# Optimization experiments

Measured on AMD Instinct MI355X. Metric: run time of the kernel, lower is better.

Reference implementation:

```python
import jax, jax.numpy as jnp
import numpy as np

N = 100000
IN_C = 128
HID = 32   # 2*out_channels
OUT = 16
NEG_SLOPE = 0.2


def gat_layer(x, src, dst, n, W, a_src, a_dst, b):
    # x: [n, Cin] -> h: [n, Cout]
    h = x @ W
    alpha_s = h @ a_src  # [n]
    alpha_d = h @ a_dst  # [n]
    e = jax.nn.leaky_relu(alpha_s[src] + alpha_d[dst], NEG_SLOPE)  # [E]
    # softmax over edges grouped by destination node (self-loops ensure no empty groups)
    m = jax.ops.segment_max(e, dst, num_segments=n)
    ex = jnp.exp(e - m[dst])
    s = jax.ops.segment_sum(ex, dst, num_segments=n)
    alpha = ex / s[dst]  # [E]
    out = jax.ops.segment_sum(h[src] * alpha[:, None], dst, num_segments=n)
    return out + b


def setup_inputs() -> dict:
    key = jax.random.key(0)
    ks = jax.random.split(key, 16)
    x = jax.random.normal(ks[0], (N, IN_C), dtype=jnp.float32)
    edge_index = jax.random.randint(ks[1], (2, 1600000), 0, N, dtype=jnp.int64)

    def glorot(k, shape):
        fan = shape[0] + (shape[1] if len(shape) > 1 else 1)
        return jax.random.normal(k, shape, dtype=jnp.float32) * jnp.sqrt(2.0 / fan)

    return {
        "x": x,
        "edge_index": edge_index,
        "W1": glorot(ks[2], (IN_C, HID)),
        "a1_src": glorot(ks[3], (HID,)),
        "a1_dst": glorot(ks[4], (HID,)),
        "b1": jnp.zeros((HID,), dtype=jnp.float32),
        "W_mu": glorot(ks[5], (HID, OUT)),
        "a_mu_src": glorot(ks[6], (OUT,)),
        "a_mu_dst": glorot(ks[7], (OUT,)),
        "b_mu": jnp.zeros((OUT,), dtype=jnp.float32),
        "W_ls": glorot(ks[8], (HID, OUT)),
        "a_ls_src": glorot(ks[9], (OUT,)),
        "a_ls_dst": glorot(ks[10], (OUT,)),
        "b_ls": jnp.zeros((OUT,), dtype=jnp.float32),
    }


def reference(x, edge_index, W1, a1_src, a1_dst, b1,
              W_mu, a_mu_src, a_mu_dst, b_mu,
              W_ls, a_ls_src, a_ls_dst, b_ls):
    n = x.shape[0]
    # PyG GATConv default: add self-loops
    loop = jnp.arange(n, dtype=edge_index.dtype)
    src = jnp.concatenate([edge_index[0], loop])
    dst = jnp.concatenate([edge_index[1], loop])

    h = jax.nn.relu(gat_layer(x, src, dst, n, W1, a1_src, a1_dst, b1))
    mu = gat_layer(h, src, dst, n, W_mu, a_mu_src, a_mu_dst, b_mu)
    logstd = gat_layer(h, src, dst, n, W_ls, a_ls_src, a_ls_dst, b_ls)
    return (mu, logstd)
```

## Files before the change

kernel.cpp:

```cpp
#include <hip/hip_runtime.h>
#include <hip/hip_bf16.h>
#include <hip/hip_fp16.h>

typedef unsigned int u32;
typedef unsigned short u16;

__device__ __forceinline__ float lrelu(float v) {
    return v > 0.f ? v : 0.2f * v;
}

__device__ __forceinline__ float4 ldq_h16(const u16* __restrict__ row, int q) {
    uint2 u = ((const uint2*)row)[q];
    __half2 a = *(__half2*)&u.x;
    __half2 b = *(__half2*)&u.y;
    float2 fa = __half22float2(a);
    float2 fb = __half22float2(b);
    return make_float4(fa.x, fa.y, fb.x, fb.y);
}

__device__ __forceinline__ u32 pack2h(float x, float y) {
    __half2 h = __float22half2_rn(make_float2(x, y));
    return *(u32*)&h;
}

#define PCHUNK 4096
#define NW 256

__global__ __launch_bounds__(256) void partition_kernel(
    const int* __restrict__ srcI, const int* __restrict__ dstI,
    u32* __restrict__ pairs, u32* __restrict__ bcur,
    int E, int wsz, int cap)
{
    __shared__ u32 lcount[NW];
    __shared__ u32 lbase[NW];
    int t = threadIdx.x;
    int chunk = blockIdx.x * PCHUNK;
    lcount[t] = 0;
    __syncthreads();
    u32 pk[16]; int wv[16]; u32 rk[16]; bool val[16];
#pragma unroll
    for (int g = 0; g < 4; g++) {
        int i0 = chunk + g * 1024 + 4 * t;
        int4 s4, d4;
        bool v4 = (i0 + 3) < E;
        if (v4) {
            s4 = *(const int4*)&srcI[i0];
            d4 = *(const int4*)&dstI[i0];
        }
        int sv[4] = {s4.x, s4.y, s4.z, s4.w};
        int dv[4] = {d4.x, d4.y, d4.z, d4.w};
#pragma unroll
        for (int j = 0; j < 4; j++) {
            int k = g * 4 + j;
            int i = i0 + j;
            val[k] = i < E;
            if (val[k]) {
                u32 s, d;
                if (v4) { s = (u32)sv[j]; d = (u32)dv[j]; }
                else    { s = (u32)srcI[i]; d = (u32)dstI[i]; }
                wv[k] = d / (u32)wsz;
                u32 dloc = d - (u32)wv[k] * (u32)wsz;
                pk[k] = (dloc << 17) | s;
                rk[k] = atomicAdd(&lcount[wv[k]], 1u);
            }
        }
    }
    __syncthreads();
    if (lcount[t] > 0)
        lbase[t] = atomicAdd(&bcur[t], lcount[t]);
    __syncthreads();
#pragma unroll
    for (int k = 0; k < 16; k++) {
        if (val[k]) {
            u32 pos = lbase[wv[k]] + rk[k];
            if (pos < (u32)cap)
                pairs[(size_t)wv[k] * cap + pos] = pk[k];
        }
    }
}

struct GSm { float xs[64][132]; float Wl[128][32]; float asv[32], adv[32]; };
struct CSm { u32 dw[512], cw[512], ts[256], hb[512]; };

__global__ __launch_bounds__(256) void g1c_kernel(
    const float* __restrict__ x, const float* __restrict__ W,
    const float* __restrict__ a_src, const float* __restrict__ a_dst,
    u16* __restrict__ h16, float* __restrict__ as_, float* __restrict__ ad_,
    const u32* __restrict__ pairs, const u32* __restrict__ bcur,
    u32* __restrict__ rowS, u32* __restrict__ deg, int* __restrict__ srcS,
    u32* __restrict__ perm,
    int n, int wsz, int cap)
{
    __shared__ __align__(16) char smraw[sizeof(GSm)];
    int t = threadIdx.x;

    if ((int)blockIdx.x < NW) {
        CSm& s = *reinterpret_cast<CSm*>(smraw);
        int grp = blockIdx.x;
        int wlo = grp * wsz;
        int wnodes = n - wlo; if (wnodes < 0) wnodes = 0; if (wnodes > wsz) wnodes = wsz;
        u32 cnt = bcur[grp]; if (cnt > (u32)cap) cnt = (u32)cap;
        size_t base = (size_t)grp * cap;

        {
            int wlo_t = t * wsz;
            int wn_t = n - wlo_t; if (wn_t < 0) wn_t = 0; if (wn_t > wsz) wn_t = wsz;
            u32 c_t = bcur[t]; if (c_t > (u32)cap) c_t = (u32)cap;
            s.ts[t] = c_t + (u32)wn_t;
            __syncthreads();
            for (int o = 1; o < NW; o <<= 1) {
                u32 y = (t >= o) ? s.ts[t - o] : 0u;
                __syncthreads();
                s.ts[t] += y;
                __syncthreads();
            }
        }
        u32 wb = s.ts[grp] - (cnt + (u32)wnodes);
        __syncthreads();

        s.dw[t] = 0; s.dw[t + 256] = 0;
        s.hb[t] = 0; s.hb[t + 256] = 0;
        __syncthreads();
        for (u32 i = t; i < cnt; i += 256)
            atomicAdd(&s.dw[pairs[base + i] >> 17], 1u);
        __syncthreads();

        int i0 = 2 * t, i1 = 2 * t + 1;
        u32 e0 = (i0 < wnodes) ? s.dw[i0] + 1u : 0u;
        u32 e1 = (i1 < wnodes) ? s.dw[i1] + 1u : 0u;
        s.ts[t] = e0 + e1;
        __syncthreads();
        for (int o = 1; o < 256; o <<= 1) {
            u32 y = (t >= o) ? s.ts[t - o] : 0u;
            __syncthreads();
            s.ts[t] += y;
            __syncthreads();
        }
        u32 off = wb + s.ts[t] - (e0 + e1);
        if (i0 < wnodes) {
            u32 dgi = s.dw[i0];
            s.cw[i0] = off;
            rowS[wlo + i0] = off;
            deg[wlo + i0] = dgi;
            srcS[off + dgi] = wlo + i0;
        }
        u32 off1 = off + e0;
        if (i1 < wnodes) {
            u32 dgi = s.dw[i1];
            s.cw[i1] = off1;
            rowS[wlo + i1] = off1;
            deg[wlo + i1] = dgi;
            srcS[off1 + dgi] = wlo + i1;
        }
        __syncthreads();

        for (int i = t; i < wnodes; i += 256)
            atomicAdd(&s.hb[s.dw[i] < 511u ? s.dw[i] : 511u], 1u);
        __syncthreads();
        {
            u32 h0 = s.hb[2 * t], h1 = s.hb[2 * t + 1];
            s.ts[t] = h0 + h1;
            __syncthreads();
            for (int o = 1; o < 256; o <<= 1) {
                u32 y = (t >= o) ? s.ts[t - o] : 0u;
                __syncthreads();
                s.ts[t] += y;
                __syncthreads();
            }
            u32 b0 = s.ts[t] - (h0 + h1);
            s.hb[2 * t] = b0;
            s.hb[2 * t + 1] = b0 + h0;
        }
        __syncthreads();
        for (int i = t; i < wnodes; i += 256) {
            u32 dg = s.dw[i] < 511u ? s.dw[i] : 511u;
            u32 pos = atomicAdd(&s.hb[dg], 1u);
            perm[wlo + pos] = (u32)(wlo + i);
        }
        for (int i = wnodes + t; i < wsz; i += 256)
            perm[wlo + i] = 0x7fffffffu;
        __syncthreads();

        for (u32 i = t; i < cnt; i += 256) {
            u32 pr = pairs[base + i];
            u32 pos = atomicAdd(&s.cw[pr >> 17], 1u);
            srcS[pos] = (int)(pr & 0x1FFFFu);
        }
        return;
    }

    GSm& s = *reinterpret_cast<GSm*>(smraw);
    int rb = (blockIdx.x - NW) * 64;

    for (int i = t; i < 4096; i += 256) s.Wl[i >> 5][i & 31] = W[i];
    if (t < 32) { s.asv[t] = a_src[t]; s.adv[t] = a_dst[t]; }
    for (int i = t; i < 2048; i += 256) {
        int row = i >> 5, seg = i & 31;
        float4 v = make_float4(0.f, 0.f, 0.f, 0.f);
        if (rb + row < n)
            v = ((const float4*)(x + (size_t)(rb + row) * 128))[seg];
        int c = seg * 4;
        s.xs[row][c + 0] = v.x; s.xs[row][c + 1] = v.y;
        s.xs[row][c + 2] = v.z; s.xs[row][c + 3] = v.w;
    }
    __syncthreads();

    int tr = t >> 3;
    int tc = t & 7;
    float acc[2][4];
#pragma unroll
    for (int i = 0; i < 2; i++)
#pragma unroll
        for (int j = 0; j < 4; j++) acc[i][j] = 0.f;

#pragma unroll 4
    for (int k = 0; k < 128; k++) {
        float x0 = s.xs[tr][k];
        float x1 = s.xs[tr + 32][k];
        float4 wv = *(const float4*)&s.Wl[k][tc * 4];
        acc[0][0] += x0 * wv.x; acc[0][1] += x0 * wv.y;
        acc[0][2] += x0 * wv.z; acc[0][3] += x0 * wv.w;
        acc[1][0] += x1 * wv.x; acc[1][1] += x1 * wv.y;
        acc[1][2] += x1 * wv.z; acc[1][3] += x1 * wv.w;
    }

#pragma unroll
    for (int i = 0; i < 2; i++) {
        int r = rb + tr + i * 32;
        if (r < n) {
            uint2 p;
            p.x = pack2h(acc[i][0], acc[i][1]);
            p.y = pack2h(acc[i][2], acc[i][3]);
            *(uint2*)&h16[(size_t)r * 32 + tc * 4] = p;
        }
        float ps = 0.f, pd = 0.f;
#pragma unroll
        for (int j = 0; j < 4; j++) {
            int c = tc * 4 + j;
            ps += acc[i][j] * s.asv[c];
            pd += acc[i][j] * s.adv[c];
        }
        for (int m = 1; m < 8; m <<= 1) {
            ps += __shfl_xor(ps, m, 64);
            pd += __shfl_xor(pd, m, 64);
        }
        if (tc == 0 && r < n) { as_[r] = ps; ad_[r] = pd; }
    }
}

__global__ __launch_bounds__(256) void l1g2_kernel(
    const u32* __restrict__ rowS, const u32* __restrict__ deg,
    const int* __restrict__ srcS, const u32* __restrict__ perm,
    const float* __restrict__ as_, const float* __restrict__ ad_,
    const u16* __restrict__ h16, const float* __restrict__ b1,
    const float* __restrict__ Wm, const float* __restrict__ Wl_,
    const float* __restrict__ ams, const float* __restrict__ amd,
    const float* __restrict__ alsb, const float* __restrict__ ald,
    u16* __restrict__ hmhl16, float2* __restrict__ attn2,
    float* __restrict__ amud, float* __restrict__ alsd,
    int n, int ntot)
{
    __shared__ float hs[16][36];
    __shared__ float Wms[32][16], Wls[32][16];
    __shared__ float amsv[16], amdv[16], alsv[16], aldv[16];
    __shared__ int dsl[16];
    int t = threadIdx.x;

    for (int i = t; i < 512; i += 256) {
        Wms[i >> 4][i & 15] = Wm[i];
        Wls[i >> 4][i & 15] = Wl_[i];
    }
    if (t < 16) {
        amsv[t] = ams[t]; amdv[t] = amd[t];
        alsv[t] = alsb[t]; aldv[t] = ald[t];
    }

    int gid = blockIdx.x * 16 + (t >> 4);
    int d = (gid < ntot) ? (int)perm[gid] : 0x7fffffff;
    bool live = (u32)d < (u32)n;
    int l  = t & 15;
    int e2 = l >> 3;
    int q  = l & 7;
    int gb = (t & 63) & 48;

    int beg = 0, end = 0;
    float adv = 0.f;
    if (live) {
        beg = (int)rowS[d];
        end = beg + (int)deg[d] + 1;
        adv = ad_[d];
    }

    float wsum = 0.f;
    float4 acc = make_float4(0.f, 0.f, 0.f, 0.f);

    int tb = beg;
    int full_end = beg + ((end - beg) & ~15);
    for (; tb < full_end; tb += 16) {
        int s = srcS[tb + l];
        float p = __expf(fminf(lrelu(as_[s] + adv), 60.f));
#pragma unroll
        for (int jj = 0; jj < 16; jj += 2) {
            int idx = jj + e2;
            int sj  = __shfl(s, gb + idx, 64);
            float w = __shfl(p, gb + idx, 64);
            wsum += w;
            float4 hv = ldq_h16(h16 + (size_t)sj * 32, q);
            acc.x += w * hv.x; acc.y += w * hv.y;
            acc.z += w * hv.z; acc.w += w * hv.w;
        }
    }
    if (tb < end) {
        int j = tb + l;
        bool valid = j < end;
        int s = valid ? srcS[j] : 0;
        float p = valid ? __expf(fminf(lrelu(as_[s] + adv), 60.f)) : 0.f;
        int cnt = end - tb;
        for (int jj = 0; jj < cnt; jj += 2) {
            int idx = jj + e2;
            int sj  = __shfl(s, gb + idx, 64);
            float w = __shfl(p, gb + idx, 64);
            if (idx >= cnt) w = 0.f;
            wsum += w;
            float4 hv = ldq_h16(h16 + (size_t)sj * 32, q);
            acc.x += w * hv.x; acc.y += w * hv.y;
            acc.z += w * hv.z; acc.w += w * hv.w;
        }
    }
    wsum  += __shfl_xor(wsum, 8, 64);
    acc.x += __shfl_xor(acc.x, 8, 64);
    acc.y += __shfl_xor(acc.y, 8, 64);
    acc.z += __shfl_xor(acc.z, 8, 64);
    acc.w += __shfl_xor(acc.w, 8, 64);

    if (l == 0) dsl[t >> 4] = live ? d : -1;
    if (live && l < 8) {
        float inv = 1.f / wsum;
        float4 r;
        r.x = fmaxf(acc.x * inv + b1[4 * q + 0], 0.f);
        r.y = fmaxf(acc.y * inv + b1[4 * q + 1], 0.f);
        r.z = fmaxf(acc.z * inv + b1[4 * q + 2], 0.f);
        r.w = fmaxf(acc.w * inv + b1[4 * q + 3], 0.f);
        *(float4*)&hs[t >> 4][4 * q] = r;
    }
    __syncthreads();

    int tr = t >> 4;
    int c  = t & 15;
    int r2 = dsl[tr];
    float accm = 0.f, accl = 0.f;
#pragma unroll
    for (int k = 0; k < 32; k++) {
        float hv = hs[tr][k];
        accm += hv * Wms[k][c];
        accl += hv * Wls[k][c];
    }
    if (r2 >= 0) {
        hmhl16[(size_t)r2 * 32 + c]      = __half_as_ushort(__float2half(accm));
        hmhl16[(size_t)r2 * 32 + 16 + c] = __half_as_ushort(__float2half(accl));
    }
    float pms = accm * amsv[c], pmd = accm * amdv[c];
    float pls = accl * alsv[c], pld = accl * aldv[c];
    for (int m = 1; m < 16; m <<= 1) {
        pms += __shfl_xor(pms, m, 64);
        pmd += __shfl_xor(pmd, m, 64);
        pls += __shfl_xor(pls, m, 64);
        pld += __shfl_xor(pld, m, 64);
    }
    if (c == 0 && r2 >= 0) {
        attn2[r2] = make_float2(pms, pls);
        amud[r2] = pmd;
        alsd[r2] = pld;
    }
}

__global__ __launch_bounds__(256) void l2_fused_kernel(
    const u32* __restrict__ rowS, const u32* __restrict__ deg,
    const int* __restrict__ srcS, const u32* __restrict__ perm,
    const float2* __restrict__ attn2,
    const float* __restrict__ amud, const float* __restrict__ alsd,
    const u16* __restrict__ hmhl16,
    const float* __restrict__ bm, const float* __restrict__ bl,
    float* __restrict__ out, int n, int ntot)
{
    int gid = blockIdx.x * 16 + (threadIdx.x >> 4);
    if (gid >= ntot) return;
    int d = (int)perm[gid];
    if (d >= n) return;
    int l  = threadIdx.x & 15;
    int e2 = l >> 3;
    int q  = l & 7;
    int gb = (threadIdx.x & 63) & 48;
    bool isMu = q < 4;

    int beg = (int)rowS[d];
    int end = beg + (int)deg[d] + 1;
    float amdv = amud[d], aldv = alsd[d];

    float wsum = 0.f;
    float4 acc = make_float4(0.f, 0.f, 0.f, 0.f);

    int tb = beg;
    int full_end = beg + ((end - beg) & ~15);
    for (; tb < full_end; tb += 16) {
        int s = srcS[tb + l];
        float2 a2 = attn2[s];
        float pm = __expf(fminf(lrelu(a2.x + amdv), 60.f));
        float pl = __expf(fminf(lrelu(a2.y + aldv), 60.f));
#pragma unroll
        for (int jj = 0; jj < 16; jj += 2) {
            int idx = jj + e2;
            int sj    = __shfl(s, gb + idx, 64);
            float pmj = __shfl(pm, gb + idx, 64);
            float plj = __shfl(pl, gb + idx, 64);
            float w = isMu ? pmj : plj;
            wsum += w;
            float4 hv = ldq_h16(hmhl16 + (size_t)sj * 32, q);
            acc.x += w * hv.x; acc.y += w * hv.y;
            acc.z += w * hv.z; acc.w += w * hv.w;
        }
    }
    if (tb < end) {
        int j = tb + l;
        bool valid = j < end;
        int s = valid ? srcS[j] : 0;
        float2 a2 = valid ? attn2[s] : make_float2(0.f, 0.f);
        float pm = valid ? __expf(fminf(lrelu(a2.x + amdv), 60.f)) : 0.f;
        float pl = valid ? __expf(fminf(lrelu(a2.y + aldv), 60.f)) : 0.f;
        int cnt = end - tb;
        for (int jj = 0; jj < cnt; jj += 2) {
            int idx = jj + e2;
            int sj    = __shfl(s, gb + idx, 64);
            float pmj = __shfl(pm, gb + idx, 64);
            float plj = __shfl(pl, gb + idx, 64);
            float w = isMu ? pmj : plj;
            if (idx >= cnt) w = 0.f;
            wsum += w;
            float4 hv = ldq_h16(hmhl16 + (size_t)sj * 32, q);
            acc.x += w * hv.x; acc.y += w * hv.y;
            acc.z += w * hv.z; acc.w += w * hv.w;
        }
    }
    wsum  += __shfl_xor(wsum, 8, 64);
    acc.x += __shfl_xor(acc.x, 8, 64);
    acc.y += __shfl_xor(acc.y, 8, 64);
    acc.z += __shfl_xor(acc.z, 8, 64);
    acc.w += __shfl_xor(acc.w, 8, 64);
    if (l < 8) {
        float inv = 1.f / wsum;
        if (q < 4) {
            float4 r;
            r.x = acc.x * inv + bm[4 * q + 0];
            r.y = acc.y * inv + bm[4 * q + 1];
            r.z = acc.z * inv + bm[4 * q + 2];
            r.w = acc.w * inv + bm[4 * q + 3];
            *(float4*)&out[(size_t)d * 16 + 4 * q] = r;
        } else {
            int qc = 4 * (q - 4);
            float4 r;
            r.x = acc.x * inv + bl[qc + 0];
            r.y = acc.y * inv + bl[qc + 1];
            r.z = acc.z * inv + bl[qc + 2];
            r.w = acc.w * inv + bl[qc + 3];
            *(float4*)&out[(size_t)n * 16 + (size_t)d * 16 + qc] = r;
        }
    }
}

extern "C" void kernel_launch(void* const* d_in, const int* in_sizes, int n_in,
                              void* d_out, int out_size, void* d_ws, size_t ws_size,
                              hipStream_t stream)
{
    const float* x   = (const float*)d_in[0];
    const int*   ei  = (const int*)d_in[1];
    const float* W1  = (const float*)d_in[2];
    const float* a1s = (const float*)d_in[3];
    const float* a1d = (const float*)d_in[4];
    const float* b1  = (const float*)d_in[5];
    const float* Wm  = (const float*)d_in[6];
    const float* ams = (const float*)d_in[7];
    const float* amd = (const float*)d_in[8];
    const float* bm  = (const float*)d_in[9];
    const float* Wl  = (const float*)d_in[10];
    const float* als = (const float*)d_in[11];
    const float* ald = (const float*)d_in[12];
    const float* bl  = (const float*)d_in[13];

    int n  = in_sizes[0] / 128;
    int E  = in_sizes[1] / 2;
    int Et = E + n;
    int wsz = (n + NW - 1) / NW;
    int cap = E / NW + 3072;
    int ntot = NW * wsz;
    const int* srcI = ei;
    const int* dstI = ei + E;

    float* ws = (float*)d_ws;
    u16*    h16   = (u16*)ws;
    u16*    hmhl16 = (u16*)(ws + (size_t)16 * n);
    u32*    pairs = (u32*)(ws + (size_t)32 * n);
    float2* attn2 = (float2*)(ws + (size_t)64 * n);
    float*  amud = ws + (size_t)66 * n;
    float*  alsd = ws + (size_t)67 * n;
    u32*    deg  = (u32*)(ws + (size_t)68 * n);
    u32*    bcur = (u32*)(ws + (size_t)69 * n);
    u32*    rowS = (u32*)(ws + (size_t)70 * n);
    int*    srcS = (int*)(ws + (size_t)71 * n);
    u32*    perm = (u32*)(ws + (size_t)71 * n + Et);
    float*  as_  = ws + (size_t)71 * n + Et + ntot;
    float*  ad_  = as_ + n;

    int pgrid = (E + PCHUNK - 1) / PCHUNK;
    int gblocks = (n + 63) / 64;

    hipMemsetAsync(bcur, 0, NW * sizeof(u32), stream);

    partition_kernel<<<pgrid, 256, 0, stream>>>(srcI, dstI, pairs, bcur,
                                                E, wsz, cap);

    g1c_kernel<<<NW + gblocks, 256, 0, stream>>>(
        x, W1, a1s, a1d, h16, as_, ad_,
        pairs, bcur, rowS, deg, srcS, perm, n, wsz, cap);

    l1g2_kernel<<<(ntot + 15) / 16, 256, 0, stream>>>(
        rowS, deg, srcS, perm, as_, ad_, h16, b1,
        Wm, Wl, ams, amd, als, ald,
        hmhl16, attn2, amud, alsd, n, ntot);

    l2_fused_kernel<<<(ntot + 15) / 16, 256, 0, stream>>>(rowS, deg, srcS, perm,
                                                          attn2, amud, alsd,
                                                          hmhl16, bm, bl,
                                                          (float*)d_out, n, ntot);
}
```

Baseline: 235.8 us.

## Split fp16 feature rows into two half-width planes gathered in separate passes

Node features are stored as two planes of 16 halves (32 bytes) each instead of one 64-byte row. The aggregation kernels now gather each plane in its own pass over the edge list, with 4 edges in flight per 16-lane group instead of 2. The aim is to shrink the gather working set per pass so it stays in cache and to improve gather parallelism. In exchange, the edge indices and attention exponentials are read and recomputed twice, and the cross-lane reductions get longer.

Measured after the change: 264.3 us. 12.1% more time.

```diff
diff --git a/kernel.cpp b/kernel.cpp
--- a/kernel.cpp
+++ b/kernel.cpp
@@ -85,7 +85,8 @@
 __global__ __launch_bounds__(256) void g1c_kernel(
     const float* __restrict__ x, const float* __restrict__ W,
     const float* __restrict__ a_src, const float* __restrict__ a_dst,
-    u16* __restrict__ h16, float* __restrict__ as_, float* __restrict__ ad_,
+    u16* __restrict__ hA, u16* __restrict__ hB,
+    float* __restrict__ as_, float* __restrict__ ad_,
     const u32* __restrict__ pairs, const u32* __restrict__ bcur,
     u32* __restrict__ rowS, u32* __restrict__ deg, int* __restrict__ srcS,
     u32* __restrict__ perm,
@@ -231,7 +232,8 @@
             uint2 p;
             p.x = pack2h(acc[i][0], acc[i][1]);
             p.y = pack2h(acc[i][2], acc[i][3]);
-            *(uint2*)&h16[(size_t)r * 32 + tc * 4] = p;
+            u16* plane = (tc < 4) ? hA : hB;
+            *(uint2*)&plane[(size_t)r * 16 + (tc & 3) * 4] = p;
         }
         float ps = 0.f, pd = 0.f;
 #pragma unroll
@@ -252,11 +254,12 @@
     const u32* __restrict__ rowS, const u32* __restrict__ deg,
     const int* __restrict__ srcS, const u32* __restrict__ perm,
     const float* __restrict__ as_, const float* __restrict__ ad_,
-    const u16* __restrict__ h16, const float* __restrict__ b1,
+    const u16* __restrict__ hA, const u16* __restrict__ hB,
+    const float* __restrict__ b1,
     const float* __restrict__ Wm, const float* __restrict__ Wl_,
     const float* __restrict__ ams, const float* __restrict__ amd,
     const float* __restrict__ alsb, const float* __restrict__ ald,
-    u16* __restrict__ hmhl16, float2* __restrict__ attn2,
+    u16* __restrict__ hmu, u16* __restrict__ hls, float2* __restrict__ attn2,
     float* __restrict__ amud, float* __restrict__ alsd,
     int n, int ntot)
 {
@@ -279,8 +282,8 @@
     int d = (gid < ntot) ? (int)perm[gid] : 0x7fffffff;
     bool live = (u32)d < (u32)n;
     int l  = t & 15;
-    int e2 = l >> 3;
-    int q  = l & 7;
+    int e4 = l >> 2;
+    int q4 = l & 3;
     int gb = (t & 63) & 48;
 
     int beg = 0, end = 0;
@@ -290,24 +293,25 @@
         end = beg + (int)deg[d] + 1;
         adv = ad_[d];
     }
+    int full_end = beg + ((end - beg) & ~15);
 
     float wsum = 0.f;
-    float4 acc = make_float4(0.f, 0.f, 0.f, 0.f);
+    float4 accA = make_float4(0.f, 0.f, 0.f, 0.f);
+    float4 accB = make_float4(0.f, 0.f, 0.f, 0.f);
 
     int tb = beg;
-    int full_end = beg + ((end - beg) & ~15);
     for (; tb < full_end; tb += 16) {
         int s = srcS[tb + l];
         float p = __expf(fminf(lrelu(as_[s] + adv), 60.f));
 #pragma unroll
-        for (int jj = 0; jj < 16; jj += 2) {
-            int idx = jj + e2;
+        for (int jj = 0; jj < 16; jj += 4) {
+            int idx = jj + e4;
             int sj  = __shfl(s, gb + idx, 64);
             float w = __shfl(p, gb + idx, 64);
             wsum += w;
-            float4 hv = ldq_h16(h16 + (size_t)sj * 32, q);
-            acc.x += w * hv.x; acc.y += w * hv.y;
-            acc.z += w * hv.z; acc.w += w * hv.w;
+            float4 hv = ldq_h16(hA + (size_t)sj * 16, q4);
+            accA.x += w * hv.x; accA.y += w * hv.y;
+            accA.z += w * hv.z; accA.w += w * hv.w;
         }
     }
     if (tb < end) {
@@ -316,32 +320,75 @@
         int s = valid ? srcS[j] : 0;
         float p = valid ? __expf(fminf(lrelu(as_[s] + adv), 60.f)) : 0.f;
         int cnt = end - tb;
-        for (int jj = 0; jj < cnt; jj += 2) {
-            int idx = jj + e2;
+        for (int jj = 0; jj < cnt; jj += 4) {
+            int idx = jj + e4;
             int sj  = __shfl(s, gb + idx, 64);
             float w = __shfl(p, gb + idx, 64);
             if (idx >= cnt) w = 0.f;
             wsum += w;
-            float4 hv = ldq_h16(h16 + (size_t)sj * 32, q);
-            acc.x += w * hv.x; acc.y += w * hv.y;
-            acc.z += w * hv.z; acc.w += w * hv.w;
-        }
-    }
-    wsum  += __shfl_xor(wsum, 8, 64);
-    acc.x += __shfl_xor(acc.x, 8, 64);
-    acc.y += __shfl_xor(acc.y, 8, 64);
-    acc.z += __shfl_xor(acc.z, 8, 64);
-    acc.w += __shfl_xor(acc.w, 8, 64);
+            float4 hv = ldq_h16(hA + (size_t)sj * 16, q4);
+            accA.x += w * hv.x; accA.y += w * hv.y;
+            accA.z += w * hv.z; accA.w += w * hv.w;
+        }
+    }
+    tb = beg;
+    for (; tb < full_end; tb += 16) {
+        int s = srcS[tb + l];
+        float p = __expf(fminf(lrelu(as_[s] + adv), 60.f));
+#pragma unroll
+        for (int jj = 0; jj < 16; jj += 4) {
+            int idx = jj + e4;
+            int sj  = __shfl(s, gb + idx, 64);
+            float w = __shfl(p, gb + idx, 64);
+            float4 hv = ldq_h16(hB + (size_t)sj * 16, q4);
+            accB.x += w * hv.x; accB.y += w * hv.y;
+            accB.z += w * hv.z; accB.w += w * hv.w;
+        }
+    }
+    if (tb < end) {
+        int j = tb + l;
+        bool valid = j < end;
+        int s = valid ? srcS[j] : 0;
+        float p = valid ? __expf(fminf(lrelu(as_[s] + adv), 60.f)) : 0.f;
+        int cnt = end - tb;
+        for (int jj = 0; jj < cnt; jj += 4) {
+            int idx = jj + e4;
+            int sj  = __shfl(s, gb + idx, 64);
+            float w = __shfl(p, gb + idx, 64);
+            if (idx >= cnt) w = 0.f;
+            float4 hv = ldq_h16(hB + (size_t)sj * 16, q4);
+            accB.x += w * hv.x; accB.y += w * hv.y;
+            accB.z += w * hv.z; accB.w += w * hv.w;
+        }
+    }
+
+#pragma unroll
+    for (int o = 4; o <= 8; o <<= 1) {
+        wsum  += __shfl_xor(wsum, o, 64);
+        accA.x += __shfl_xor(accA.x, o, 64);
+        accA.y += __shfl_xor(accA.y, o, 64);
+        accA.z += __shfl_xor(accA.z, o, 64);
+        accA.w += __shfl_xor(accA.w, o, 64);
+        accB.x += __shfl_xor(accB.x, o, 64);
+        accB.y += __shfl_xor(accB.y, o, 64);
+        accB.z += __shfl_xor(accB.z, o, 64);
+        accB.w += __shfl_xor(accB.w, o, 64);
+    }
 
     if (l == 0) dsl[t >> 4] = live ? d : -1;
-    if (live && l < 8) {
+    if (live && l < 4) {
         float inv = 1.f / wsum;
-        float4 r;
-        r.x = fmaxf(acc.x * inv + b1[4 * q + 0], 0.f);
-        r.y = fmaxf(acc.y * inv + b1[4 * q + 1], 0.f);
-        r.z = fmaxf(acc.z * inv + b1[4 * q + 2], 0.f);
-        r.w = fmaxf(acc.w * inv + b1[4 * q + 3], 0.f);
-        *(float4*)&hs[t >> 4][4 * q] = r;
+        float4 rA, rB;
+        rA.x = fmaxf(accA.x * inv + b1[4 * q4 + 0], 0.f);
+        rA.y = fmaxf(accA.y * inv + b1[4 * q4 + 1], 0.f);
+        rA.z = fmaxf(accA.z * inv + b1[4 * q4 + 2], 0.f);
+        rA.w = fmaxf(accA.w * inv + b1[4 * q4 + 3], 0.f);
+        rB.x = fmaxf(accB.x * inv + b1[16 + 4 * q4 + 0], 0.f);
+        rB.y = fmaxf(accB.y * inv + b1[16 + 4 * q4 + 1], 0.f);
+        rB.z = fmaxf(accB.z * inv + b1[16 + 4 * q4 + 2], 0.f);
+        rB.w = fmaxf(accB.w * inv + b1[16 + 4 * q4 + 3], 0.f);
+        *(float4*)&hs[t >> 4][4 * q4]      = rA;
+        *(float4*)&hs[t >> 4][16 + 4 * q4] = rB;
     }
     __syncthreads();
 
@@ -356,8 +403,8 @@
         accl += hv * Wls[k][c];
     }
     if (r2 >= 0) {
-        hmhl16[(size_t)r2 * 32 + c]      = __half_as_ushort(__float2half(accm));
-        hmhl16[(size_t)r2 * 32 + 16 + c] = __half_as_ushort(__float2half(accl));
+        hmu[(size_t)r2 * 16 + c] = __half_as_ushort(__float2half(accm));
+        hls[(size_t)r2 * 16 + c] = __half_as_ushort(__float2half(accl));
     }
     float pms = accm * amsv[c], pmd = accm * amdv[c];
     float pls = accl * alsv[c], pld = accl * aldv[c];
@@ -379,7 +426,7 @@
     const int* __restrict__ srcS, const u32* __restrict__ perm,
     const float2* __restrict__ attn2,
     const float* __restrict__ amud, const float* __restrict__ alsd,
-    const u16* __restrict__ hmhl16,
+    const u16* __restrict__ hmu, const u16* __restrict__ hls,
     const float* __restrict__ bm, const float* __restrict__ bl,
     float* __restrict__ out, int n, int ntot)
 {
@@ -388,82 +435,111 @@
     int d = (int)perm[gid];
     if (d >= n) return;
     int l  = threadIdx.x & 15;
-    int e2 = l >> 3;
-    int q  = l & 7;
+    int e4 = l >> 2;
+    int q4 = l & 3;
     int gb = (threadIdx.x & 63) & 48;
-    bool isMu = q < 4;
 
     int beg = (int)rowS[d];
     int end = beg + (int)deg[d] + 1;
+    int full_end = beg + ((end - beg) & ~15);
     float amdv = amud[d], aldv = alsd[d];
 
-    float wsum = 0.f;
-    float4 acc = make_float4(0.f, 0.f, 0.f, 0.f);
+    float wsm = 0.f, wsl = 0.f;
+    float4 accm = make_float4(0.f, 0.f, 0.f, 0.f);
+    float4 accl = make_float4(0.f, 0.f, 0.f, 0.f);
 
     int tb = beg;
-    int full_end = beg + ((end - beg) & ~15);
     for (; tb < full_end; tb += 16) {
         int s = srcS[tb + l];
-        float2 a2 = attn2[s];
-        float pm = __expf(fminf(lrelu(a2.x + amdv), 60.f));
-        float pl = __expf(fminf(lrelu(a2.y + aldv), 60.f));
-#pragma unroll
-        for (int jj = 0; jj < 16; jj += 2) {
-            int idx = jj + e2;
-            int sj    = __shfl(s, gb + idx, 64);
-            float pmj = __shfl(pm, gb + idx, 64);
-            float plj = __shfl(pl, gb + idx, 64);
-            float w = isMu ? pmj : plj;
-            wsum += w;
-            float4 hv = ldq_h16(hmhl16 + (size_t)sj * 32, q);
-            acc.x += w * hv.x; acc.y += w * hv.y;
-            acc.z += w * hv.z; acc.w += w * hv.w;
+        float pm = __expf(fminf(lrelu(attn2[s].x + amdv), 60.f));
+#pragma unroll
+        for (int jj = 0; jj < 16; jj += 4) {
+            int idx = jj + e4;
+            int sj  = __shfl(s, gb + idx, 64);
+            float w = __shfl(pm, gb + idx, 64);
+            wsm += w;
+            float4 hv = ldq_h16(hmu + (size_t)sj * 16, q4);
+            accm.x += w * hv.x; accm.y += w * hv.y;
+            accm.z += w * hv.z; accm.w += w * hv.w;
         }
     }
     if (tb < end) {
         int j = tb + l;
         bool valid = j < end;
         int s = valid ? srcS[j] : 0;
-        float2 a2 = valid ? attn2[s] : make_float2(0.f, 0.f);
-        float pm = valid ? __expf(fminf(lrelu(a2.x + amdv), 60.f)) : 0.f;
-        float pl = valid ? __expf(fminf(lrelu(a2.y + aldv), 60.f)) : 0.f;
+        float pm = valid ? __expf(fminf(lrelu(attn2[s].x + amdv), 60.f)) : 0.f;
         int cnt = end - tb;
-        for (int jj = 0; jj < cnt; jj += 2) {
-            int idx = jj + e2;
-            int sj    = __shfl(s, gb + idx, 64);
-            float pmj = __shfl(pm, gb + idx, 64);
-            float plj = __shfl(pl, gb + idx, 64);
-            float w = isMu ? pmj : plj;
+        for (int jj = 0; jj < cnt; jj += 4) {
+            int idx = jj + e4;
+            int sj  = __shfl(s, gb + idx, 64);
+            float w = __shfl(pm, gb + idx, 64);
             if (idx >= cnt) w = 0.f;
-            wsum += w;
-            float4 hv = ldq_h16(hmhl16 + (size_t)sj * 32, q);
-            acc.x += w * hv.x; acc.y += w * hv.y;
-            acc.z += w * hv.z; acc.w += w * hv.w;
-        }
-    }
-    wsum  += __shfl_xor(wsum, 8, 64);
-    acc.x += __shfl_xor(acc.x, 8, 64);
-    acc.y += __shfl_xor(acc.y, 8, 64);
-    acc.z += __shfl_xor(acc.z, 8, 64);
-    acc.w += __shfl_xor(acc.w, 8, 64);
-    if (l < 8) {
-        float inv = 1.f / wsum;
-        if (q < 4) {
-            float4 r;
-            r.x = acc.x * inv + bm[4 * q + 0];
-            r.y = acc.y * inv + bm[4 * q + 1];
-            r.z = acc.z * inv + bm[4 * q + 2];
-            r.w = acc.w * inv + bm[4 * q + 3];
-            *(float4*)&out[(size_t)d * 16 + 4 * q] = r;
-        } else {
-            int qc = 4 * (q - 4);
-            float4 r;
-            r.x = acc.x * inv + bl[qc + 0];
-            r.y = acc.y * inv + bl[qc + 1];
-            r.z = acc.z * inv + bl[qc + 2];
-            r.w = acc.w * inv + bl[qc + 3];
-            *(float4*)&out[(size_t)n * 16 + (size_t)d * 16 + qc] = r;
-        }
+            wsm += w;
+            float4 hv = ldq_h16(hmu + (size_t)sj * 16, q4);
+            accm.x += w * hv.x; accm.y += w * hv.y;
+            accm.z += w * hv.z; accm.w += w * hv.w;
+        }
+    }
+    tb = beg;
+    for (; tb < full_end; tb += 16) {
+        int s = srcS[tb + l];
+        float pl = __expf(fminf(lrelu(attn2[s].y + aldv), 60.f));
+#pragma unroll
+        for (int jj = 0; jj < 16; jj += 4) {
+            int idx = jj + e4;
+            int sj  = __shfl(s, gb + idx, 64);
+            float w = __shfl(pl, gb + idx, 64);
+            wsl += w;
+            float4 hv = ldq_h16(hls + (size_t)sj * 16, q4);
+            accl.x += w * hv.x; accl.y += w * hv.y;
+            accl.z += w * hv.z; accl.w += w * hv.w;
+        }
+    }
+    if (tb < end) {
+        int j = tb + l;
+        bool valid = j < end;
+        int s = valid ? srcS[j] : 0;
+        float pl = valid ? __expf(fminf(lrelu(attn2[s].y + aldv), 60.f)) : 0.f;
+        int cnt = end - tb;
+        for (int jj = 0; jj < cnt; jj += 4) {
+            int idx = jj + e4;
+            int sj  = __shfl(s, gb + idx, 64);
+            float w = __shfl(pl, gb + idx, 64);
+            if (idx >= cnt) w = 0.f;
+            wsl += w;
+            float4 hv = ldq_h16(hls + (size_t)sj * 16, q4);
+            accl.x += w * hv.x; accl.y += w * hv.y;
+            accl.z += w * hv.z; accl.w += w * hv.w;
+        }
+    }
+
+#pragma unroll
+    for (int o = 4; o <= 8; o <<= 1) {
+        wsm   += __shfl_xor(wsm, o, 64);
+        wsl   += __shfl_xor(wsl, o, 64);
+        accm.x += __shfl_xor(accm.x, o, 64);
+        accm.y += __shfl_xor(accm.y, o, 64);
+        accm.z += __shfl_xor(accm.z, o, 64);
+        accm.w += __shfl_xor(accm.w, o, 64);
+        accl.x += __shfl_xor(accl.x, o, 64);
+        accl.y += __shfl_xor(accl.y, o, 64);
+        accl.z += __shfl_xor(accl.z, o, 64);
+        accl.w += __shfl_xor(accl.w, o, 64);
+    }
+    if (l < 4) {
+        float invm = 1.f / wsm;
+        float invl = 1.f / wsl;
+        float4 rm, rl;
+        rm.x = accm.x * invm + bm[4 * q4 + 0];
+        rm.y = accm.y * invm + bm[4 * q4 + 1];
+        rm.z = accm.z * invm + bm[4 * q4 + 2];
+        rm.w = accm.w * invm + bm[4 * q4 + 3];
+        rl.x = accl.x * invl + bl[4 * q4 + 0];
+        rl.y = accl.y * invl + bl[4 * q4 + 1];
+        rl.z = accl.z * invl + bl[4 * q4 + 2];
+        rl.w = accl.w * invl + bl[4 * q4 + 3];
+        *(float4*)&out[(size_t)d * 16 + 4 * q4] = rm;
+        *(float4*)&out[(size_t)n * 16 + (size_t)d * 16 + 4 * q4] = rl;
     }
 }
 
@@ -496,8 +572,10 @@
     const int* dstI = ei + E;
 
     float* ws = (float*)d_ws;
-    u16*    h16   = (u16*)ws;
-    u16*    hmhl16 = (u16*)(ws + (size_t)16 * n);
+    u16*    hA   = (u16*)ws;
+    u16*    hB   = (u16*)(ws + (size_t)8 * n);
+    u16*    hmu  = (u16*)(ws + (size_t)16 * n);
+    u16*    hls  = (u16*)(ws + (size_t)24 * n);
     u32*    pairs = (u32*)(ws + (size_t)32 * n);
     float2* attn2 = (float2*)(ws + (size_t)64 * n);
     float*  amud = ws + (size_t)66 * n;
@@ -519,16 +597,16 @@
                                                 E, wsz, cap);
 
     g1c_kernel<<<NW + gblocks, 256, 0, stream>>>(
-        x, W1, a1s, a1d, h16, as_, ad_,
+        x, W1, a1s, a1d, hA, hB, as_, ad_,
         pairs, bcur, rowS, deg, srcS, perm, n, wsz, cap);
 
     l1g2_kernel<<<(ntot + 15) / 16, 256, 0, stream>>>(
-        rowS, deg, srcS, perm, as_, ad_, h16, b1,
+        rowS, deg, srcS, perm, as_, ad_, hA, hB, b1,
         Wm, Wl, ams, amd, als, ald,
-        hmhl16, attn2, amud, alsd, n, ntot);
+        hmu, hls, attn2, amud, alsd, n, ntot);
 
     l2_fused_kernel<<<(ntot + 15) / 16, 256, 0, stream>>>(rowS, deg, srcS, perm,
                                                           attn2, amud, alsd,
-                                                          hmhl16, bm, bl,
+                                                          hmu, hls, bm, bl,
                                                           (float*)d_out, n, ntot);
 }
```
